# Kernel optimization log

Hardware: AMD Instinct MI355X
Metric: run time of the kernel (lower is better)

Reference implementation:

```python
import jax, jax.numpy as jnp
import numpy as np

# Standard Human3.6M 17-joint skeleton parents; CHILD_JOINTS[j] = children of joint j.
_PARENTS = np.array([-1, 0, 1, 2, 0, 4, 5, 0, 7, 8, 9, 8, 11, 12, 8, 14, 15])
_J = 17

def _child_mean_matrix():
    """[J,J] matrix M s.t. child_feat = M @ x_joints reproduces the per-joint
    child-mean gather loop (identity row for leaf joints)."""
    M = np.zeros((_J, _J), dtype=np.float32)
    for j in range(_J):
        ch = [i for i in range(_J) if _PARENTS[i] == j]
        if ch:
            M[j, ch] = 1.0 / len(ch)
        else:
            M[j, j] = 1.0
    return M

_CHILD_M = _child_mean_matrix()

B, N, J, C = 8, 243, 17, 512
H = 8
D = C // H

def setup_inputs() -> dict:
    key = jax.random.key(0)
    ks = jax.random.split(key, 9)
    s = 0.02
    return {
        "x": jax.random.normal(ks[0], (B, N, J, C), dtype=jnp.float32),
        "W_qkv": jax.random.normal(ks[1], (C, 3 * C), dtype=jnp.float32) * s,
        "b_qkv": jnp.zeros((3 * C,), dtype=jnp.float32),
        "W_q": jax.random.normal(ks[2], (C, C), dtype=jnp.float32) * s,
        "b_q": jnp.zeros((C,), dtype=jnp.float32),
        "W_kv": jax.random.normal(ks[3], (C, 2 * C), dtype=jnp.float32) * s,
        "b_kv": jnp.zeros((2 * C,), dtype=jnp.float32),
        "W_proj": jax.random.normal(ks[4], (C, C), dtype=jnp.float32) * s,
        "b_proj": jnp.zeros((C,), dtype=jnp.float32),
    }

def _attn(q, k, v, scale):
    # q,k,v: [B,J,N,H,D]; attention over temporal axis N per (b,j,h)
    a = jnp.einsum('bjnhd,bjmhd->bjhnm', q, k) * scale
    a = jax.nn.softmax(a, axis=-1)
    return jnp.einsum('bjhnm,bjmhd->bjnhd', a, v)

def reference(x, W_qkv, b_qkv, W_q, b_q, W_kv, b_kv, W_proj, b_proj):
    Bx, Nx, Jx, Cx = x.shape
    scale = 1.0 / jnp.sqrt(jnp.asarray(D, x.dtype))
    Mchild = jnp.asarray(_CHILD_M, x.dtype)

    xt = jnp.transpose(x, (0, 2, 1, 3))  # [B,J,N,C] -> per-(b,j) temporal sequences

    # Temporal self-attention (TSA)
    qkv = (xt @ W_qkv + b_qkv).reshape(Bx, Jx, Nx, 3, H, D)
    q_t, k_t, v_t = qkv[:, :, :, 0], qkv[:, :, :, 1], qkv[:, :, :, 2]
    x_tsa = _attn(q_t, k_t, v_t, scale).reshape(Bx, Jx, Nx, Cx)

    # Hierarchical temporal cross-attention (HTC): K/V from child-joint mean
    child = jnp.einsum('jk,bknc->bjnc', Mchild, xt)  # [B,J,N,C]
    q_h = (xt @ W_q + b_q).reshape(Bx, Jx, Nx, H, D)
    kv = (child @ W_kv + b_kv).reshape(Bx, Jx, Nx, 2, H, D)
    k_h, v_h = kv[:, :, :, 0], kv[:, :, :, 1]
    x_htc = _attn(q_h, k_h, v_h, scale).reshape(Bx, Jx, Nx, Cx)

    # Fuse, project, residual + LayerNorm (no affine; dropout is identity in eval)
    fuse = jnp.transpose(x_tsa + x_htc, (0, 2, 1, 3))  # [B,N,J,C]
    fuse = fuse @ W_proj + b_proj
    y = x + fuse
    mu = jnp.mean(y, axis=-1, keepdims=True)
    var = jnp.var(y, axis=-1, keepdims=True)
    return (y - mu) / jnp.sqrt(var + 1e-5)
```

## Files before the change

### kernel.cpp

```cpp
#include <hip/hip_runtime.h>

typedef unsigned short u16;
typedef unsigned int u32;
typedef __attribute__((ext_vector_type(8))) short bf16x8;
typedef __attribute__((ext_vector_type(8))) u16  u16x8;
typedef __attribute__((ext_vector_type(4))) float f32x4;

#define TOK   33048
#define NSEQ  243
#define TE    16920576u
#define GSTR  15552
#define VTP   256

__device__ __forceinline__ float bf2f(u16 u){
    union { unsigned int i; float f; } v; v.i = ((unsigned int)u) << 16; return v.f;
}
__device__ __forceinline__ u16 f2bf(float f){
    union { float f; unsigned int i; } v; v.f = f;
    unsigned int r = v.i + 0x7fffu + ((v.i >> 16) & 1u);
    return (u16)(r >> 16);
}

__device__ __forceinline__ void gload_lds16(const void* g, void* l){
    __builtin_amdgcn_global_load_lds(
        (const __attribute__((address_space(1))) unsigned int*)g,
        (__attribute__((address_space(3))) unsigned int*)l, 16, 0, 0);
}

__global__ __launch_bounds__(256) void k_cvt_xbf(const float* __restrict__ x, u16* __restrict__ xbf){
    int idx = blockIdx.x*256 + threadIdx.x;
    int t  = idx >> 6;
    int c8 = (idx & 63) << 3;
    unsigned b   = (unsigned)t / 4131u;
    unsigned rem = (unsigned)t % 4131u;
    unsigned j = rem / 243u, n = rem % 243u;
    const float* src = x + ((size_t)(b*243u + n)*17u + j)*512u + c8;
    f32x4 a = *(const f32x4*)src;
    f32x4 c = *(const f32x4*)(src+4);
    u16x8 o;
    #pragma unroll
    for (int e=0;e<4;e++){ o[e]=f2bf(a[e]); o[e+4]=f2bf(c[e]); }
    *(u16x8*)(xbf + (size_t)t*512 + c8) = o;
}

__global__ __launch_bounds__(256) void k_cvt_wcat(const float* __restrict__ Wqkv,
                                                  const float* __restrict__ Wq,
                                                  const float* __restrict__ Wkv,
                                                  u16* __restrict__ WcatT){
    int idx = blockIdx.x*256 + threadIdx.x;
    int k  = idx / 384;
    int c0 = (idx % 384) * 8;
    const float* src;
    if (c0 < 1536)      src = Wqkv + (size_t)k*1536 + c0;
    else if (c0 < 2048) src = Wq   + (size_t)k*512  + (c0 - 1536);
    else                src = Wkv  + (size_t)k*1024 + (c0 - 2048);
    f32x4 a = *(const f32x4*)src;
    f32x4 b = *(const f32x4*)(src+4);
    #pragma unroll
    for (int e=0;e<4;e++){
        WcatT[(size_t)(c0+e)*512 + k]   = f2bf(a[e]);
        WcatT[(size_t)(c0+4+e)*512 + k] = f2bf(b[e]);
    }
}

__global__ __launch_bounds__(256) void k_cvt_wproj(const float* __restrict__ Wp, u16* __restrict__ WpT){
    int idx = blockIdx.x*256 + threadIdx.x;
    int k  = idx / 64;
    int c0 = (idx % 64) * 8;
    f32x4 a = *(const f32x4*)(Wp + (size_t)k*512 + c0);
    f32x4 b = *(const f32x4*)(Wp + (size_t)k*512 + c0 + 4);
    #pragma unroll
    for (int e=0;e<4;e++){
        WpT[(size_t)(c0+e)*512 + k]   = f2bf(a[e]);
        WpT[(size_t)(c0+4+e)*512 + k] = f2bf(b[e]);
    }
}

__global__ __launch_bounds__(256) void k_gemm_in(
    const u16* __restrict__ xbf, const u16* __restrict__ WcatT,
    const float* __restrict__ b_qkv, const float* __restrict__ b_q,
    const float* __restrict__ b_kv, u16* __restrict__ ws3, int c_off)
{
    __shared__ __align__(16) u16 smem[32768];

    const int orig = blockIdx.x;
    const int xcd  = orig & 7;
    const int wg   = (xcd < 4 ? xcd*389 : 4*389 + (xcd-4)*388) + (orig >> 3);
    const int nt = wg % 12, mt = wg / 12;

    const int tid = threadIdx.x;
    const int w = tid >> 6, lane = tid & 63;
    const int wm = w >> 1, wn = w & 1;
    const int lg = lane >> 4, li = lane & 15;
    const int x7 = li & 7;

    const int sr8  = lane >> 3;
    const int schx = (lane & 7) ^ sr8;
    const u16* gA = xbf   + (size_t)(mt*128 + w*32 + sr8)*512 + schx*8;
    const u16* gB = WcatT + (size_t)(c_off + nt*128 + w*32 + sr8)*512 + schx*8;

    f32x4 acc[4][4];
    #pragma unroll
    for (int i=0;i<4;i++)
        #pragma unroll
        for (int jj=0;jj<4;jj++){ acc[i][jj][0]=0.f; acc[i][jj][1]=0.f; acc[i][jj][2]=0.f; acc[i][jj][3]=0.f; }

    #pragma unroll
    for (int i=0;i<4;i++){
        gload_lds16(gA + i*4096, smem + (w*32 + i*8)*64);
        gload_lds16(gB + i*4096, smem + 8192 + (w*32 + i*8)*64);
    }
    __syncthreads();

    int cur = 0;
    #pragma unroll
    for (int k0 = 0; k0 < 512; k0 += 64){
        if (k0 < 448){
            u16* nb = smem + (cur^1)*16384;
            #pragma unroll
            for (int i=0;i<4;i++){
                gload_lds16(gA + i*4096 + k0 + 64, nb + (w*32 + i*8)*64);
                gload_lds16(gB + i*4096 + k0 + 64, nb + 8192 + (w*32 + i*8)*64);
            }
        }
        const u16* As = smem + cur*16384;
        const u16* Bs = As + 8192;
        #pragma unroll
        for (int ks=0; ks<2; ks++){
            bf16x8 av[4], bv[4];
            #pragma unroll
            for (int mf=0;mf<4;mf++){
                const int R = wm*64 + mf*16 + li;
                av[mf] = *(const bf16x8*)&As[R*64 + (((ks*4+lg) ^ x7)*8)];
            }
            #pragma unroll
            for (int nf=0;nf<4;nf++){
                const int R = wn*64 + nf*16 + li;
                bv[nf] = *(const bf16x8*)&Bs[R*64 + (((ks*4+lg) ^ x7)*8)];
            }
            #pragma unroll
            for (int mf=0;mf<4;mf++)
                #pragma unroll
                for (int nf=0;nf<4;nf++)
                    acc[mf][nf] = __builtin_amdgcn_mfma_f32_16x16x32_bf16(av[mf], bv[nf], acc[mf][nf], 0, 0, 0);
        }
        __syncthreads();
        cur ^= 1;
    }

    float bias[4];
    #pragma unroll
    for (int nf=0;nf<4;nf++){
        const int c = c_off + nt*128 + wn*64 + nf*16 + li;
        bias[nf] = (c < 1536) ? b_qkv[c] : (c < 2048 ? b_q[c-1536] : b_kv[c-2048]);
    }

    u16* L = smem + w*1152;
    const int colbase = nt*128 + wn*64;
    const int slot = colbase >> 9;
    const float osc = (slot == 0) ? 0.125f : 1.0f;
    const int hh   = (colbase >> 6) & 7;
    const int rloc = lane & 15;
    const int cchunk = lane >> 4;
    const int dd = (colbase + cchunk*8) & 63;
    u16* tbase = ws3 + (size_t)slot * TE;
    u16* vt    = ws3 + (size_t)2 * TE;

    #pragma unroll
    for (int mf=0;mf<4;mf++){
        __syncthreads();
        #pragma unroll
        for (int nf=0;nf<4;nf++)
            #pragma unroll
            for (int reg=0;reg<4;reg++)
                L[(lg*4+reg)*72 + nf*16 + li] = f2bf((acc[mf][nf][reg] + bias[nf]) * osc);
        __syncthreads();
        const int rr_base = mt*128 + wm*64 + mf*16;
        if (slot < 2){
            const int rr = rr_base + rloc;
            if (rr < TOK){
                u16x8 v0 = *(const u16x8*)&L[rloc*72 + cchunk*8];
                u16x8 v1 = *(const u16x8*)&L[rloc*72 + 32 + cchunk*8];
                const unsigned bj = (unsigned)rr / 243u;
                const unsigned n  = (unsigned)rr % 243u;
                u16* dst = tbase + ((size_t)(bj*8u + hh)*243u + n)*64u + dd;
                *(u16x8*)dst      = v0;
                *(u16x8*)(dst+32) = v1;
            }
        } else {
            u16 colv[16];
            #pragma unroll
            for (int r=0;r<16;r++) colv[r] = L[r*72 + lane];
            if (rr_base < TOK){
                const unsigned bj0 = (unsigned)rr_base / 243u;
                const unsigned n0  = (unsigned)rr_base % 243u;
                if (n0 <= 227 && rr_base + 15 < TOK){
                    u16x8 vlo, vhi;
                    #pragma unroll
                    for (int e=0;e<8;e++){ vlo[e]=colv[e]; vhi[e]=colv[e+8]; }
                    u16* dst = vt + ((size_t)(bj0*8u + hh)*64u + lane)*VTP + n0;
                    *(u16x8*)dst     = vlo;
                    *(u16x8*)(dst+8) = vhi;
                } else {
                    for (int r=0;r<16;r++){
                        const int rr = rr_base + r;
                        if (rr < TOK){
                            const unsigned bjr = (unsigned)rr / 243u;
                            const unsigned nr  = (unsigned)rr % 243u;
                            vt[((size_t)(bjr*8u + hh)*64u + lane)*VTP + nr] = colv[r];
                        }
                    }
                }
            }
        }
    }
}

__constant__ int g_child[17][3] = {
  {1,4,7},{2,-1,-1},{3,-1,-1},{3,-1,-1},{5,-1,-1},{6,-1,-1},{6,-1,-1},{8,-1,-1},
  {9,11,14},{10,-1,-1},{10,-1,-1},{12,-1,-1},{13,-1,-1},{13,-1,-1},{15,-1,-1},
  {16,-1,-1},{16,-1,-1}};
__constant__ float g_cw[17] = {0.33333333f,1,1,1,1,1,1,1,0.33333333f,1,1,1,1,1,1,1,1};

__global__ __launch_bounds__(256) void k_mixk(const u16* __restrict__ Kraw, u16* __restrict__ Kmix){
    const int c = blockIdx.x*256 + threadIdx.x;
    const int g = c / 1944;
    const int off = (c % 1944) * 8;
    const int bj = g >> 3, h = g & 7;
    const int b_ = bj / 17, j_ = bj % 17;
    const float wgt = g_cw[j_];
    float acc[8];
    #pragma unroll
    for (int e=0;e<8;e++) acc[e]=0.f;
    #pragma unroll
    for (int ci=0;ci<3;ci++){
        const int cj = g_child[j_][ci];
        if (cj >= 0){
            const u16x8 v = *(const u16x8*)(Kraw + (size_t)((b_*17+cj)*8+h)*GSTR + off);
            #pragma unroll
            for (int e=0;e<8;e++) acc[e] += wgt*bf2f(v[e]);
        }
    }
    u16x8 o;
    #pragma unroll
    for (int e=0;e<8;e++) o[e]=f2bf(acc[e]);
    *(u16x8*)(Kmix + (size_t)g*GSTR + off) = o;
}

__global__ __launch_bounds__(256) void k_mixv(const u16* __restrict__ VTraw, u16* __restrict__ VTmix){
    const int c = blockIdx.x*256 + threadIdx.x;
    const int g = c / 2048;
    const int off = (c % 2048) * 8;
    const int bj = g >> 3, h = g & 7;
    const int b_ = bj / 17, j_ = bj % 17;
    const float wgt = g_cw[j_];
    float acc[8];
    #pragma unroll
    for (int e=0;e<8;e++) acc[e]=0.f;
    #pragma unroll
    for (int ci=0;ci<3;ci++){
        const int cj = g_child[j_][ci];
        if (cj >= 0){
            const u16x8 v = *(const u16x8*)(VTraw + (size_t)((b_*17+cj)*8+h)*16384u + off);
            #pragma unroll
            for (int e=0;e<8;e++) acc[e] += wgt*bf2f(v[e]);
        }
    }
    u16x8 o;
    #pragma unroll
    for (int e=0;e<8;e++) o[e]=f2bf(acc[e]);
    *(u16x8*)(VTmix + (size_t)g*16384u + off) = o;
}

__global__ __launch_bounds__(256, 3) void k_attn(
    const u16* __restrict__ Qb, const u16* __restrict__ Kb,
    const u16* __restrict__ VTb, u16* __restrict__ attn, int rmw)
{
    __shared__ __align__(16) u16 smem[16384];

    const int orig = blockIdx.x;
    const int xcd  = orig & 7;
    const int lin  = orig >> 3;
    const int p2   = lin & 1;
    const int g    = (lin >> 1)*8 + xcd;
    const int bj = g >> 3, h = g & 7;

    const int tid = threadIdx.x, lane = tid & 63, w = tid >> 6;
    const int lg = lane >> 4, li = lane & 15;

    const int qrowA = p2*128 + w*16;
    const int qrowB = qrowA + 64;
    bf16x8 qA0 = {0,0,0,0,0,0,0,0}, qA1 = qA0, qB0 = qA0, qB1 = qA0;
    {
        const int qrA = qrowA + li;
        const u16* qp = Qb + (size_t)g*GSTR + (size_t)qrA*64;
        qA0 = *(const bf16x8*)(qp + lg*8);
        qA1 = *(const bf16x8*)(qp + 32 + lg*8);
        const int qrB = qrowB + li;
        if (qrB < NSEQ){
            const u16* qp2 = Qb + (size_t)g*GSTR + (size_t)qrB*64;
            qB0 = *(const bf16x8*)(qp2 + lg*8);
            qB1 = *(const bf16x8*)(qp2 + 32 + lg*8);
        }
    }

    const int schx = (lane & 7) ^ (lane >> 3);
    const u16* ksrc = Kb  + (size_t)g*GSTR   + (size_t)(w*16 + (lane>>3))*64  + schx*8;
    const u16* vsrc = VTb + (size_t)g*16384u + (size_t)(w*16 + (lane>>3))*VTP + schx*8;

    const int laneA = li + 32*(lg & 1);
    const int laneB = laneA + 16;
    const bool sel = (lg >> 1) != 0;
    const int x7 = li & 7;

    float sumA = 0.f, sumB = 0.f;
    f32x4 oA[4], oB[4];
    #pragma unroll
    for (int dn=0;dn<4;dn++){
        oA[dn][0]=0.f; oA[dn][1]=0.f; oA[dn][2]=0.f; oA[dn][3]=0.f;
        oB[dn][0]=0.f; oB[dn][1]=0.f; oB[dn][2]=0.f; oB[dn][3]=0.f;
    }

    {
        char* b0 = (char*)smem;
        gload_lds16(ksrc,         b0 + w*2048);
        gload_lds16(ksrc + 512,   b0 + w*2048 + 1024);
        gload_lds16(vsrc,         b0 + 8192 + w*2048);
        gload_lds16(vsrc + 8*VTP, b0 + 8192 + w*2048 + 1024);
    }
    __syncthreads();

    int cur = 0;
    #pragma unroll
    for (int t=0; t<4; t++){
        if (t < 3){
            char* nb = (char*)smem + (cur^1)*16384;
            gload_lds16(ksrc + (size_t)(t+1)*4096,        nb + w*2048);
            gload_lds16(ksrc + (size_t)(t+1)*4096 + 512,  nb + w*2048 + 1024);
            gload_lds16(vsrc + (t+1)*64,                  nb + 8192 + w*2048);
            gload_lds16(vsrc + (t+1)*64 + 8*VTP,          nb + 8192 + w*2048 + 1024);
        }
        char* kl = (char*)smem + cur*16384;
        char* vl = kl + 8192;

        #pragma unroll
        for (int half=0; half<2; half++){
            u32 lo2A[2], hi2A[2], lo2B[2], hi2B[2];
            #pragma unroll
            for (int t2=0; t2<2; t2++){
                const int nt2l = half*2 + t2;
                const int row  = nt2l*16 + li;
                const bf16x8 kb0 = *(const bf16x8*)(kl + row*128 + (((lg  ) ^ x7)<<4));
                const bf16x8 kb1 = *(const bf16x8*)(kl + row*128 + (((4+lg) ^ x7)<<4));
                f32x4 sA; sA[0]=0.f; sA[1]=0.f; sA[2]=0.f; sA[3]=0.f;
                f32x4 sB = sA;
                sA = __builtin_amdgcn_mfma_f32_16x16x32_bf16(kb0, qA0, sA, 0,0,0);
                sA = __builtin_amdgcn_mfma_f32_16x16x32_bf16(kb1, qA1, sA, 0,0,0);
                sB = __builtin_amdgcn_mfma_f32_16x16x32_bf16(kb0, qB0, sB, 0,0,0);
                sB = __builtin_amdgcn_mfma_f32_16x16x32_bf16(kb1, qB1, sB, 0,0,0);
                if (t == 3 && nt2l == 3){
                    sA[3] = -1e30f; sB[3] = -1e30f;
                    if (lg){ sA[0]=-1e30f; sA[1]=-1e30f; sA[2]=-1e30f;
                             sB[0]=-1e30f; sB[1]=-1e30f; sB[2]=-1e30f; }
                }
                const float a0 = __expf(sA[0]);
                const float a1 = __expf(sA[1]);
                const float a2 = __expf(sA[2]);
                const float a3 = __expf(sA[3]);
                sumA += (a0+a1)+(a2+a3);
                lo2A[t2] = (u32)f2bf(a0) | ((u32)f2bf(a1) << 16);
                hi2A[t2] = (u32)f2bf(a2) | ((u32)f2bf(a3) << 16);
                const float b0 = __expf(sB[0]);
                const float b1 = __expf(sB[1]);
                const float b2 = __expf(sB[2]);
                const float b3 = __expf(sB[3]);
                sumB += (b0+b1)+(b2+b3);
                lo2B[t2] = (u32)f2bf(b0) | ((u32)f2bf(b1) << 16);
                hi2B[t2] = (u32)f2bf(b2) | ((u32)f2bf(b3) << 16);
            }
            bf16x8 paA, paB;
            {
                u32 a0 = __shfl((int)lo2A[0], laneA), a1 = __shfl((int)lo2A[1], laneA);
                u32 b0 = __shfl((int)hi2A[0], laneA), b1 = __shfl((int)hi2A[1], laneA);
                u32 c0 = __shfl((int)lo2A[0], laneB), c1 = __shfl((int)lo2A[1], laneB);
                u32 d0 = __shfl((int)hi2A[0], laneB), d1 = __shfl((int)hi2A[1], laneB);
                union { u32 u[4]; bf16x8 v; } pk;
                pk.u[0] = sel ? a1 : a0;
                pk.u[1] = sel ? b1 : b0;
                pk.u[2] = sel ? c1 : c0;
                pk.u[3] = sel ? d1 : d0;
                paA = pk.v;
            }
            {
                u32 a0 = __shfl((int)lo2B[0], laneA), a1 = __shfl((int)lo2B[1], laneA);
                u32 b0 = __shfl((int)hi2B[0], laneA), b1 = __shfl((int)hi2B[1], laneA);
                u32 c0 = __shfl((int)lo2B[0], laneB), c1 = __shfl((int)lo2B[1], laneB);
                u32 d0 = __shfl((int)hi2B[0], laneB), d1 = __shfl((int)hi2B[1], laneB);
                union { u32 u[4]; bf16x8 v; } pk;
                pk.u[0] = sel ? a1 : a0;
                pk.u[1] = sel ? b1 : b0;
                pk.u[2] = sel ? c1 : c0;
                pk.u[3] = sel ? d1 : d0;
                paB = pk.v;
            }
            #pragma unroll
            for (int dn=0;dn<4;dn++){
                const int d = dn*16 + li;
                const bf16x8 vb = *(const bf16x8*)(vl + d*128 + ((((half<<2)+lg) ^ x7)<<4));
                oA[dn] = __builtin_amdgcn_mfma_f32_16x16x32_bf16(paA, vb, oA[dn], 0,0,0);
                oB[dn] = __builtin_amdgcn_mfma_f32_16x16x32_bf16(paB, vb, oB[dn], 0,0,0);
            }
        }
        __syncthreads();
        cur ^= 1;
    }

    sumA += __shfl_xor(sumA,16); sumA += __shfl_xor(sumA,32);
    sumB += __shfl_xor(sumB,16); sumB += __shfl_xor(sumB,32);
    const float invA = 1.f/sumA;
    const float invB = 1.f/sumB;
    float invrA[4], invrB[4];
    #pragma unroll
    for (int r=0;r<4;r++){
        invrA[r] = __shfl(invA, lg*4+r);
        invrB[r] = __shfl(invB, lg*4+r);
    }

    #pragma unroll
    for (int dn=0;dn<4;dn++){
        #pragma unroll
        for (int r=0;r<4;r++){
            const int qrow = qrowA + lg*4 + r;
            const size_t off = ((size_t)bj*243 + qrow)*512 + h*64 + dn*16 + li;
            float val = oA[dn][r] * invrA[r];
            if (rmw) val += bf2f(attn[off]);
            attn[off] = f2bf(val);
        }
        #pragma unroll
        for (int r=0;r<4;r++){
            const int qrow = qrowB + lg*4 + r;
            if (qrow < NSEQ){
                const size_t off = ((size_t)bj*243 + qrow)*512 + h*64 + dn*16 + li;
                float val = oB[dn][r] * invrB[r];
                if (rmw) val += bf2f(attn[off]);
                attn[off] = f2bf(val);
            }
        }
    }
}

__global__ __launch_bounds__(256) void k_gemm_proj(
    const u16* __restrict__ attnb, const u16* __restrict__ WprojT,
    const float* __restrict__ b_proj, float* __restrict__ fuse)
{
    __shared__ __align__(16) u16 smem[32768];

    const int orig = blockIdx.x;
    const int xcd  = orig & 7;
    const int wg   = (xcd < 4 ? xcd*130 : 4*130 + (xcd-4)*129) + (orig >> 3);
    const int nt = wg & 3, mt = wg >> 2;

    const int tid = threadIdx.x;
    const int w = tid >> 6, lane = tid & 63;
    const int wm = w >> 1, wn = w & 1;
    const int lg = lane >> 4, li = lane & 15;
    const int x7 = li & 7;

    const int sr8  = lane >> 3;
    const int schx = (lane & 7) ^ sr8;
    const u16* gA = attnb  + (size_t)(mt*128 + w*32 + sr8)*512 + schx*8;
    const u16* gB = WprojT + (size_t)(nt*128 + w*32 + sr8)*512 + schx*8;

    f32x4 acc[4][4];
    #pragma unroll
    for (int i=0;i<4;i++)
        #pragma unroll
        for (int jj=0;jj<4;jj++){ acc[i][jj][0]=0.f; acc[i][jj][1]=0.f; acc[i][jj][2]=0.f; acc[i][jj][3]=0.f; }

    #pragma unroll
    for (int i=0;i<4;i++){
        gload_lds16(gA + i*4096, smem + (w*32 + i*8)*64);
        gload_lds16(gB + i*4096, smem + 8192 + (w*32 + i*8)*64);
    }
    __syncthreads();

    int cur = 0;
    #pragma unroll
    for (int k0 = 0; k0 < 512; k0 += 64){
        if (k0 < 448){
            u16* nb = smem + (cur^1)*16384;
            #pragma unroll
            for (int i=0;i<4;i++){
                gload_lds16(gA + i*4096 + k0 + 64, nb + (w*32 + i*8)*64);
                gload_lds16(gB + i*4096 + k0 + 64, nb + 8192 + (w*32 + i*8)*64);
            }
        }
        const u16* As = smem + cur*16384;
        const u16* Bs = As + 8192;
        #pragma unroll
        for (int ks=0; ks<2; ks++){
            bf16x8 av[4], bv[4];
            #pragma unroll
            for (int mf=0;mf<4;mf++){
                const int R = wm*64 + mf*16 + li;
                av[mf] = *(const bf16x8*)&As[R*64 + (((ks*4+lg) ^ x7)*8)];
            }
            #pragma unroll
            for (int nf=0;nf<4;nf++){
                const int R = wn*64 + nf*16 + li;
                bv[nf] = *(const bf16x8*)&Bs[R*64 + (((ks*4+lg) ^ x7)*8)];
            }
            #pragma unroll
            for (int mf=0;mf<4;mf++)
                #pragma unroll
                for (int nf=0;nf<4;nf++)
                    acc[mf][nf] = __builtin_amdgcn_mfma_f32_16x16x32_bf16(av[mf], bv[nf], acc[mf][nf], 0, 0, 0);
        }
        __syncthreads();
        cur ^= 1;
    }

    #pragma unroll
    for (int mf=0;mf<4;mf++)
        #pragma unroll
        for (int reg=0;reg<4;reg++){
            const int rr = mt*128 + wm*64 + mf*16 + lg*4 + reg;
            if (rr < TOK){
                #pragma unroll
                for (int nf=0;nf<4;nf++){
                    const int c = nt*128 + wn*64 + nf*16 + li;
                    fuse[(size_t)rr*512 + c] = acc[mf][nf][reg] + b_proj[c];
                }
            }
        }
}

__global__ __launch_bounds__(256) void k_ln(
    const float* __restrict__ x, const float* __restrict__ fuse, float* __restrict__ out)
{
    const int w = threadIdx.x >> 6, lane = threadIdx.x & 63;
    const int o = blockIdx.x*4 + w;
    const unsigned b_  = (unsigned)o / 4131u;
    const unsigned rem = (unsigned)o % 4131u;
    const unsigned n = rem / 17u, j = rem % 17u;
    const unsigned t = (b_*17u + j)*243u + n;
    const float* fr = fuse + (size_t)t*512 + lane*8;
    const float* xr = x    + (size_t)o*512 + lane*8;
    f32x4 f0 = *(const f32x4*)fr, f1 = *(const f32x4*)(fr+4);
    f32x4 x0 = *(const f32x4*)xr, x1 = *(const f32x4*)(xr+4);
    float y[8];
    #pragma unroll
    for (int e=0;e<4;e++){ y[e] = x0[e]+f0[e]; y[e+4] = x1[e]+f1[e]; }
    float s1=0.f, s2=0.f;
    #pragma unroll
    for (int e=0;e<8;e++){ s1 += y[e]; s2 += y[e]*y[e]; }
    #pragma unroll
    for (int m=1;m<64;m<<=1){ s1 += __shfl_xor(s1,m); s2 += __shfl_xor(s2,m); }
    const float mu  = s1 * (1.f/512.f);
    const float var = s2 * (1.f/512.f) - mu*mu;
    const float rstd = rsqrtf(var + 1e-5f);
    float* orow = out + (size_t)o*512 + lane*8;
    f32x4 o0, o1;
    #pragma unroll
    for (int e=0;e<4;e++){ o0[e] = (y[e]-mu)*rstd; o1[e] = (y[e+4]-mu)*rstd; }
    *(f32x4*)orow = o0; *(f32x4*)(orow+4) = o1;
}

extern "C" void kernel_launch(void* const* d_in, const int* in_sizes, int n_in,
                              void* d_out, int out_size, void* d_ws, size_t ws_size,
                              hipStream_t stream)
{
    const float* x      = (const float*)d_in[0];
    const float* W_qkv  = (const float*)d_in[1];
    const float* b_qkv  = (const float*)d_in[2];
    const float* W_q    = (const float*)d_in[3];
    const float* b_q    = (const float*)d_in[4];
    const float* W_kv   = (const float*)d_in[5];
    const float* b_kv   = (const float*)d_in[6];
    const float* W_proj = (const float*)d_in[7];
    const float* b_proj = (const float*)d_in[8];

    char* ws = (char*)d_ws;
    u16*   xbf    = (u16*)(ws);
    u16*   kmix   = (u16*)(ws);
    u16*   ws3    = (u16*)(ws + 33972224u);
    u16*   attn   = (u16*)(ws + 137306112u);
    u16*   WcatT  = (u16*)(ws + 171278336u);
    u16*   WprojT = (u16*)(ws + 174424064u);
    u16*   vtmix  = (u16*)(ws + 174948352u);
    float* fuse   = (float*)(ws + 33972224u);
    float* out    = (float*)d_out;

    k_cvt_xbf  <<<8262, 256, 0, stream>>>(x, xbf);
    k_cvt_wcat <<<768,  256, 0, stream>>>(W_qkv, W_q, W_kv, WcatT);
    k_cvt_wproj<<<128,  256, 0, stream>>>(W_proj, WprojT);

    k_gemm_in<<<3108, 256, 0, stream>>>(xbf, WcatT, b_qkv, b_q, b_kv, ws3, 0);
    k_attn<<<2176, 256, 0, stream>>>(ws3, ws3 + (size_t)TE, ws3 + (size_t)2*TE, attn, 0);

    k_gemm_in<<<3108, 256, 0, stream>>>(xbf, WcatT, b_qkv, b_q, b_kv, ws3, 1536);
    k_mixk<<<8262, 256, 0, stream>>>(ws3 + (size_t)TE, kmix);
    k_mixv<<<8704, 256, 0, stream>>>(ws3 + (size_t)2*TE, vtmix);
    k_attn<<<2176, 256, 0, stream>>>(ws3, kmix, vtmix, attn, 1);

    k_gemm_proj<<<1036, 256, 0, stream>>>(attn, WprojT, b_proj, fuse);

    k_ln<<<8262, 256, 0, stream>>>(x, fuse, out);
}
```

Baseline: 378.7 us.

## Single-buffer GEMM LDS, fine-grained waitcnt in attention, bf16 fuse intermediate

The two GEMM kernels drop LDS double buffering in favour of a single 32KB buffer, loading each k-tile and then syncing. This halves LDS use to raise occupancy, but the load and compute phases are no longer overlapped. The attention kernel replaces its __syncthreads with explicit vmcnt waits plus raw barriers, so the prefetch of the next tile can stay in flight. The projection output is now stored as bf16 instead of fp32, which halves the fuse write and the LayerNorm read traffic at some cost in precision.

```diff
diff --git a/kernel.cpp b/kernel.cpp
--- a/kernel.cpp
+++ b/kernel.cpp
@@ -81,7 +81,7 @@
     const float* __restrict__ b_qkv, const float* __restrict__ b_q,
     const float* __restrict__ b_kv, u16* __restrict__ ws3, int c_off)
 {
-    __shared__ __align__(16) u16 smem[32768];
+    __shared__ __align__(16) u16 smem[16384];
 
     const int orig = blockIdx.x;
     const int xcd  = orig & 7;
@@ -106,25 +106,16 @@
         for (int jj=0;jj<4;jj++){ acc[i][jj][0]=0.f; acc[i][jj][1]=0.f; acc[i][jj][2]=0.f; acc[i][jj][3]=0.f; }
 
     #pragma unroll
-    for (int i=0;i<4;i++){
-        gload_lds16(gA + i*4096, smem + (w*32 + i*8)*64);
-        gload_lds16(gB + i*4096, smem + 8192 + (w*32 + i*8)*64);
-    }
-    __syncthreads();
-
-    int cur = 0;
-    #pragma unroll
     for (int k0 = 0; k0 < 512; k0 += 64){
-        if (k0 < 448){
-            u16* nb = smem + (cur^1)*16384;
-            #pragma unroll
-            for (int i=0;i<4;i++){
-                gload_lds16(gA + i*4096 + k0 + 64, nb + (w*32 + i*8)*64);
-                gload_lds16(gB + i*4096 + k0 + 64, nb + 8192 + (w*32 + i*8)*64);
-            }
-        }
-        const u16* As = smem + cur*16384;
-        const u16* Bs = As + 8192;
+        __syncthreads();
+        #pragma unroll
+        for (int i=0;i<4;i++){
+            gload_lds16(gA + i*4096 + k0, smem + (w*32 + i*8)*64);
+            gload_lds16(gB + i*4096 + k0, smem + 8192 + (w*32 + i*8)*64);
+        }
+        __syncthreads();
+        const u16* As = smem;
+        const u16* Bs = smem + 8192;
         #pragma unroll
         for (int ks=0; ks<2; ks++){
             bf16x8 av[4], bv[4];
@@ -144,8 +135,6 @@
                 for (int nf=0;nf<4;nf++)
                     acc[mf][nf] = __builtin_amdgcn_mfma_f32_16x16x32_bf16(av[mf], bv[nf], acc[mf][nf], 0, 0, 0);
         }
-        __syncthreads();
-        cur ^= 1;
     }
 
     float bias[4];
@@ -328,7 +317,6 @@
         gload_lds16(vsrc,         b0 + 8192 + w*2048);
         gload_lds16(vsrc + 8*VTP, b0 + 8192 + w*2048 + 1024);
     }
-    __syncthreads();
 
     int cur = 0;
     #pragma unroll
@@ -339,7 +327,11 @@
             gload_lds16(ksrc + (size_t)(t+1)*4096 + 512,  nb + w*2048 + 1024);
             gload_lds16(vsrc + (t+1)*64,                  nb + 8192 + w*2048);
             gload_lds16(vsrc + (t+1)*64 + 8*VTP,          nb + 8192 + w*2048 + 1024);
-        }
+            asm volatile("s_waitcnt vmcnt(4)");
+        } else {
+            asm volatile("s_waitcnt vmcnt(0)");
+        }
+        __builtin_amdgcn_s_barrier();
         char* kl = (char*)smem + cur*16384;
         char* vl = kl + 8192;
 
@@ -411,7 +403,7 @@
                 oB[dn] = __builtin_amdgcn_mfma_f32_16x16x32_bf16(paB, vb, oB[dn], 0,0,0);
             }
         }
-        __syncthreads();
+        __builtin_amdgcn_s_barrier();
         cur ^= 1;
     }
 
@@ -451,9 +443,9 @@
 
 __global__ __launch_bounds__(256) void k_gemm_proj(
     const u16* __restrict__ attnb, const u16* __restrict__ WprojT,
-    const float* __restrict__ b_proj, float* __restrict__ fuse)
+    const float* __restrict__ b_proj, u16* __restrict__ fuseb)
 {
-    __shared__ __align__(16) u16 smem[32768];
+    __shared__ __align__(16) u16 smem[16384];
 
     const int orig = blockIdx.x;
     const int xcd  = orig & 7;
@@ -478,25 +470,16 @@
         for (int jj=0;jj<4;jj++){ acc[i][jj][0]=0.f; acc[i][jj][1]=0.f; acc[i][jj][2]=0.f; acc[i][jj][3]=0.f; }
 
     #pragma unroll
-    for (int i=0;i<4;i++){
-        gload_lds16(gA + i*4096, smem + (w*32 + i*8)*64);
-        gload_lds16(gB + i*4096, smem + 8192 + (w*32 + i*8)*64);
-    }
-    __syncthreads();
-
-    int cur = 0;
-    #pragma unroll
     for (int k0 = 0; k0 < 512; k0 += 64){
-        if (k0 < 448){
-            u16* nb = smem + (cur^1)*16384;
-            #pragma unroll
-            for (int i=0;i<4;i++){
-                gload_lds16(gA + i*4096 + k0 + 64, nb + (w*32 + i*8)*64);
-                gload_lds16(gB + i*4096 + k0 + 64, nb + 8192 + (w*32 + i*8)*64);
-            }
-        }
-        const u16* As = smem + cur*16384;
-        const u16* Bs = As + 8192;
+        __syncthreads();
+        #pragma unroll
+        for (int i=0;i<4;i++){
+            gload_lds16(gA + i*4096 + k0, smem + (w*32 + i*8)*64);
+            gload_lds16(gB + i*4096 + k0, smem + 8192 + (w*32 + i*8)*64);
+        }
+        __syncthreads();
+        const u16* As = smem;
+        const u16* Bs = smem + 8192;
         #pragma unroll
         for (int ks=0; ks<2; ks++){
             bf16x8 av[4], bv[4];
@@ -516,8 +499,6 @@
                 for (int nf=0;nf<4;nf++)
                     acc[mf][nf] = __builtin_amdgcn_mfma_f32_16x16x32_bf16(av[mf], bv[nf], acc[mf][nf], 0, 0, 0);
         }
-        __syncthreads();
-        cur ^= 1;
     }
 
     #pragma unroll
@@ -529,14 +510,14 @@
                 #pragma unroll
                 for (int nf=0;nf<4;nf++){
                     const int c = nt*128 + wn*64 + nf*16 + li;
-                    fuse[(size_t)rr*512 + c] = acc[mf][nf][reg] + b_proj[c];
+                    fuseb[(size_t)rr*512 + c] = f2bf(acc[mf][nf][reg] + b_proj[c]);
                 }
             }
         }
 }
 
 __global__ __launch_bounds__(256) void k_ln(
-    const float* __restrict__ x, const float* __restrict__ fuse, float* __restrict__ out)
+    const float* __restrict__ x, const u16* __restrict__ fuseb, float* __restrict__ out)
 {
     const int w = threadIdx.x >> 6, lane = threadIdx.x & 63;
     const int o = blockIdx.x*4 + w;
@@ -544,13 +525,13 @@
     const unsigned rem = (unsigned)o % 4131u;
     const unsigned n = rem / 17u, j = rem % 17u;
     const unsigned t = (b_*17u + j)*243u + n;
-    const float* fr = fuse + (size_t)t*512 + lane*8;
-    const float* xr = x    + (size_t)o*512 + lane*8;
-    f32x4 f0 = *(const f32x4*)fr, f1 = *(const f32x4*)(fr+4);
+    const u16*   fr = fuseb + (size_t)t*512 + lane*8;
+    const float* xr = x     + (size_t)o*512 + lane*8;
+    u16x8 f = *(const u16x8*)fr;
     f32x4 x0 = *(const f32x4*)xr, x1 = *(const f32x4*)(xr+4);
     float y[8];
     #pragma unroll
-    for (int e=0;e<4;e++){ y[e] = x0[e]+f0[e]; y[e+4] = x1[e]+f1[e]; }
+    for (int e=0;e<4;e++){ y[e] = x0[e]+bf2f(f[e]); y[e+4] = x1[e]+bf2f(f[e+4]); }
     float s1=0.f, s2=0.f;
     #pragma unroll
     for (int e=0;e<8;e++){ s1 += y[e]; s2 += y[e]*y[e]; }
@@ -588,7 +569,7 @@
     u16*   WcatT  = (u16*)(ws + 171278336u);
     u16*   WprojT = (u16*)(ws + 174424064u);
     u16*   vtmix  = (u16*)(ws + 174948352u);
-    float* fuse   = (float*)(ws + 33972224u);
+    u16*   fuseb  = (u16*)(ws + 33972224u);
     float* out    = (float*)d_out;
 
     k_cvt_xbf  <<<8262, 256, 0, stream>>>(x, xbf);
@@ -603,7 +584,7 @@
     k_mixv<<<8704, 256, 0, stream>>>(ws3 + (size_t)2*TE, vtmix);
     k_attn<<<2176, 256, 0, stream>>>(ws3, kmix, vtmix, attn, 1);
 
-    k_gemm_proj<<<1036, 256, 0, stream>>>(attn, WprojT, b_proj, fuse);
-
-    k_ln<<<8262, 256, 0, stream>>>(x, fuse, out);
-}
+    k_gemm_proj<<<1036, 256, 0, stream>>>(attn, WprojT, b_proj, fuseb);
+
+    k_ln<<<8262, 256, 0, stream>>>(x, fuseb, out);
+}
```

Result: faster. 370.9 us (-2.1%).
